# Kernel tuning notes

Measured on AMD Instinct MI355X. Metric: run time of the kernel, lower is better.

## Reference

```python
import jax, jax.numpy as jnp
import numpy as np

SR = 44100.0  # sample_rate from init_kwargs


def _alpha(tau_ms):
    # Eq. (10): alpha = exp(-1 / (tau_s * fs)), tau clamped to [0.1, 1000] ms
    tau_s = jnp.clip(tau_ms, 0.1, 1000.0) / 1000.0
    return jnp.exp(-1.0 / (tau_s * SR))


def _env(x, alpha, attack):
    # Nonlinear envelope follower (Eqs. 9-10).
    # attack=True  -> smooth attack (when |x| rising), instant decay
    # attack=False -> smooth decay  (when |x| falling), instant attack
    xa = jnp.abs(x)
    xs = jnp.moveaxis(xa, -1, 0)  # [T, B, C]
    y0 = jnp.zeros(xa.shape[:-1], xa.dtype)  # [B, C]

    def step(y_prev, xn):
        cond = (xn > y_prev) if attack else (xn < y_prev)
        y_curr = jnp.where(cond, (1.0 - alpha) * xn + alpha * y_prev, xn)
        return y_curr, y_curr

    _, ys = jax.lax.scan(step, y0, xs)
    return jnp.moveaxis(ys, 0, -1)  # [B, C, T]


def _db_to_amp(db):
    return jnp.power(10.0, db / 20.0)


def reference(x, tauAtc, tauDtc, nu, dBregDelta):
    # Temporal Contrast Enhancement (Weger et al., ICAD 2019, Eqs. 12-14).
    # high_pass_filter is the identity in the source, so sh = x.
    alpha_d = _alpha(jnp.clip(tauDtc, 1.0, 100.0))
    alpha_a = _alpha(jnp.clip(tauAtc, 1.0, 100.0))
    et_d = _env(x, alpha_d, attack=False)      # envd(sh)
    et_a = _env(et_d, alpha_a, attack=True)    # enva(et_d)
    nu_amp = _db_to_amp(jnp.clip(nu, -60.0, 0.0))
    et = jnp.maximum(et_d - et_a - nu_amp, 0.0)
    et_env = _env(et, alpha_d, attack=False)   # envd(et)
    reg = _db_to_amp(jnp.clip(dBregDelta, -120.0, -60.0))
    modulation = et / (et_env + reg)
    return x * modulation


def setup_inputs() -> dict:
    key = jax.random.key(0)
    x = jax.random.normal(key, (8, 32, 88200), dtype=jnp.float32)  # [B, C, T]
    return {
        "x": x,
        "tauAtc": jnp.float32(3.0),
        "tauDtc": jnp.float32(7.0),
        "nu": jnp.float32(-40.0),
        "dBregDelta": jnp.float32(-96.0),
    }
```

## Files before the change

### kernel.cpp

```cpp
#include <hip/hip_runtime.h>
#include <cmath>


static constexpr int   kT  = 88200;
static constexpr float kSR = 44100.0f;

struct EnvP { float ad, bd, aa, ba, nuamp, reg; };

__device__ __forceinline__ EnvP make_params(const float* tauA, const float* tauD,
                                            const float* nu, const float* dbreg) {
  EnvP p;
  float td = fminf(fmaxf(tauD[0], 1.0f), 100.0f);
  td = fminf(fmaxf(td, 0.1f), 1000.0f) * 0.001f;
  float ta = fminf(fmaxf(tauA[0], 1.0f), 100.0f);
  ta = fminf(fmaxf(ta, 0.1f), 1000.0f) * 0.001f;
  p.ad = expf(-1.0f / (td * kSR));
  p.aa = expf(-1.0f / (ta * kSR));
  p.bd = 1.0f - p.ad;
  p.ba = 1.0f - p.aa;
  p.nuamp = exp10f(fminf(fmaxf(nu[0],    -60.0f),   0.0f) * 0.05f);
  p.reg   = exp10f(fminf(fmaxf(dbreg[0], -120.0f), -60.0f) * 0.05f);
  return p;
}

template <int S, int MODE>
__global__ __launch_bounds__(256)
void k_pass(const float* __restrict__ x,
            const float* tauA, const float* tauD,
            const float* nu, const float* dbreg,
            const float* __restrict__ Yd, const float* __restrict__ Ya,
            const float* __restrict__ Ye,
            float* __restrict__ O0, float* __restrict__ O1) {
  constexpr int PADS = S + 4;
  __shared__ float lds[256 * PADS];
  const int t   = threadIdx.x;
  const int blk = blockIdx.x;
  const size_t tileBase = (size_t)blk * (256 * S);
  const float4* xg = reinterpret_cast<const float4*>(x + tileBase);

#pragma unroll
  for (int i = 0; i < S / 4; ++i) {
    int idx = t + i * 256;
    float4 v = xg[idx];
    int chunk = (idx * 4) / S;
    int off   = idx * 4 - chunk * S;
    *reinterpret_cast<float4*>(&lds[chunk * PADS + off]) = v;
  }
  __syncthreads();

  EnvP p = make_params(tauA, tauD, nu, dbreg);
  const int gchunk = blk * 256 + t;
  float* my = &lds[t * PADS];

  if (MODE == 0) {
    float A = -INFINITY, B = 0.0f;
#pragma unroll 2
    for (int i = 0; i < S / 4; ++i) {
      float4 v = *reinterpret_cast<const float4*>(&my[4 * i]);
      float vv[4] = {v.x, v.y, v.z, v.w};
#pragma unroll
      for (int j = 0; j < 4; ++j) {
        float xa = fabsf(vv[j]);
        float bx = p.bd * xa;
        A = fmaxf(xa, fmaf(p.ad, A, bx));
        B = fmaf(p.ad, B, bx);
      }
    }
    O0[gchunk] = A; O1[gchunk] = B;
  } else if (MODE == 1) {
    float yd = Yd[gchunk];
    float A = INFINITY, B = 0.0f;
#pragma unroll 2
    for (int i = 0; i < S / 4; ++i) {
      float4 v = *reinterpret_cast<const float4*>(&my[4 * i]);
      float vv[4] = {v.x, v.y, v.z, v.w};
#pragma unroll
      for (int j = 0; j < 4; ++j) {
        float xa = fabsf(vv[j]);
        yd = fmaxf(xa, fmaf(p.ad, yd, p.bd * xa));
        float by = p.ba * yd;
        A = fminf(yd, fmaf(p.aa, A, by));
        B = fmaf(p.aa, B, by);
      }
    }
    O0[gchunk] = A; O1[gchunk] = B;
  } else if (MODE == 2) {
    float yd = Yd[gchunk], ya = Ya[gchunk];
    float A = -INFINITY, B = 0.0f;
#pragma unroll 2
    for (int i = 0; i < S / 4; ++i) {
      float4 v = *reinterpret_cast<const float4*>(&my[4 * i]);
      float vv[4] = {v.x, v.y, v.z, v.w};
#pragma unroll
      for (int j = 0; j < 4; ++j) {
        float xa = fabsf(vv[j]);
        yd = fmaxf(xa, fmaf(p.ad, yd, p.bd * xa));
        ya = fminf(yd, fmaf(p.aa, ya, p.ba * yd));
        float et = fmaxf((yd - ya) - p.nuamp, 0.0f);
        float bx = p.bd * et;
        A = fmaxf(et, fmaf(p.ad, A, bx));
        B = fmaf(p.ad, B, bx);
      }
    }
    O0[gchunk] = A; O1[gchunk] = B;
  } else {
    float yd = Yd[gchunk], ya = Ya[gchunk], ye = Ye[gchunk];
#pragma unroll 2
    for (int i = 0; i < S / 4; ++i) {
      float4 v = *reinterpret_cast<const float4*>(&my[4 * i]);
      float vv[4] = {v.x, v.y, v.z, v.w};
      float oo[4];
#pragma unroll
      for (int j = 0; j < 4; ++j) {
        float xa = fabsf(vv[j]);
        yd = fmaxf(xa, fmaf(p.ad, yd, p.bd * xa));
        ya = fminf(yd, fmaf(p.aa, ya, p.ba * yd));
        float et = fmaxf((yd - ya) - p.nuamp, 0.0f);
        ye = fmaxf(et, fmaf(p.ad, ye, p.bd * et));
        oo[j] = vv[j] * (et / (ye + p.reg));
      }
      *reinterpret_cast<float4*>(&my[4 * i]) = make_float4(oo[0], oo[1], oo[2], oo[3]);
    }
    __syncthreads();
    float4* og = reinterpret_cast<float4*>(O0 + tileBase);
#pragma unroll
    for (int i = 0; i < S / 4; ++i) {
      int idx = t + i * 256;
      int chunk = (idx * 4) / S;
      int off   = idx * 4 - chunk * S;
      og[idx] = *reinterpret_cast<const float4*>(&lds[chunk * PADS + off]);
    }
  }
}

template <int S, int ATTACK>
__global__ __launch_bounds__(256)
void k_scan(const float* __restrict__ A, const float* __restrict__ B,
            float* __restrict__ Y,
            const float* tauA, const float* tauD,
            const float* nu, const float* dbreg) {
  constexpr int NC  = kT / S;
  constexpr int CPT = (NC + 255) / 256;
  EnvP p = make_params(tauA, tauD, nu, dbreg);
  const float alpha = ATTACK ? p.aa : p.ad;
  const float ID_A  = ATTACK ? INFINITY : -INFINITY;
  int s = blockIdx.x, t = threadIdx.x;
  long base = (long)s * NC;
  float gS = powf(alpha, (float)S);

  float ca[CPT], cb[CPT];
  float a = ID_A, b = 0.0f, g = 1.0f;
#pragma unroll
  for (int k = 0; k < CPT; ++k) {
    int c = t * CPT + k;
    if (c < NC) { ca[k] = A[base + c]; cb[k] = B[base + c]; }
    else        { ca[k] = ID_A;        cb[k] = 0.0f; }
    float cg = (c < NC) ? gS : 1.0f;
    float na = ATTACK ? fminf(ca[k], fmaf(cg, a, cb[k]))
                      : fmaxf(ca[k], fmaf(cg, a, cb[k]));
    b = fmaf(cg, b, cb[k]);
    g = cg * g;
    a = na;
  }

  __shared__ float sA[256], sB[256], sG[256];
  sA[t] = a; sB[t] = b; sG[t] = g;
  __syncthreads();
#pragma unroll
  for (int d = 1; d < 256; d <<= 1) {
    float pa = 0.0f, pb = 0.0f, pg = 0.0f;
    if (t >= d) { pa = sA[t - d]; pb = sB[t - d]; pg = sG[t - d]; }
    __syncthreads();
    if (t >= d) {
      float na = ATTACK ? fminf(a, fmaf(g, pa, b)) : fmaxf(a, fmaf(g, pa, b));
      b = fmaf(g, pb, b);
      g = g * pg;
      a = na;
      sA[t] = a; sB[t] = b; sG[t] = g;
    }
    __syncthreads();
  }

  float ea, eb;
  if (t == 0) { ea = ID_A; eb = 0.0f; }
  else        { ea = sA[t - 1]; eb = sB[t - 1]; }

#pragma unroll
  for (int k = 0; k < CPT; ++k) {
    int c = t * CPT + k;
    if (c >= NC) break;
    Y[base + c] = ATTACK ? fminf(ea, eb) : fmaxf(ea, eb);
    float na = ATTACK ? fminf(ca[k], fmaf(gS, ea, cb[k]))
                      : fmaxf(ca[k], fmaf(gS, ea, cb[k]));
    eb = fmaf(gS, eb, cb[k]);
    ea = na;
  }
}

template <int S>
static void run_pipeline(const float* x, const float* tauA, const float* tauD,
                         const float* nu, const float* dbreg, float* out,
                         float* wsf, int nseries, hipStream_t stream) {
  const int nc  = kT / S;
  const int nch = nseries * nc;
  float* A  = wsf;
  float* B  = wsf + (size_t)nch;
  float* Yd = wsf + (size_t)2 * nch;
  float* Ya = wsf + (size_t)3 * nch;
  float* Ye = wsf + (size_t)4 * nch;
  const int grid = nch / 256;

  k_pass<S, 0><<<grid, 256, 0, stream>>>(x, tauA, tauD, nu, dbreg, nullptr, nullptr, nullptr, A, B);
  k_scan<S, 0><<<nseries, 256, 0, stream>>>(A, B, Yd, tauA, tauD, nu, dbreg);
  k_pass<S, 1><<<grid, 256, 0, stream>>>(x, tauA, tauD, nu, dbreg, Yd, nullptr, nullptr, A, B);
  k_scan<S, 1><<<nseries, 256, 0, stream>>>(A, B, Ya, tauA, tauD, nu, dbreg);
  k_pass<S, 2><<<grid, 256, 0, stream>>>(x, tauA, tauD, nu, dbreg, Yd, Ya, nullptr, A, B);
  k_scan<S, 0><<<nseries, 256, 0, stream>>>(A, B, Ye, tauA, tauD, nu, dbreg);
  k_pass<S, 3><<<grid, 256, 0, stream>>>(x, tauA, tauD, nu, dbreg, Yd, Ya, Ye, out, nullptr);
}

extern "C" void kernel_launch(void* const* d_in, const int* in_sizes, int n_in,
                              void* d_out, int out_size, void* d_ws, size_t ws_size,
                              hipStream_t stream) {
  const float* x     = (const float*)d_in[0];
  const float* tauA  = (const float*)d_in[1];
  const float* tauD  = (const float*)d_in[2];
  const float* nu    = (const float*)d_in[3];
  const float* dbreg = (const float*)d_in[4];
  float* out = (float*)d_out;
  float* wsf = (float*)d_ws;
  int nseries = in_sizes[0] / kT;

  auto fits = [&](int S) {
    return (size_t)5 * nseries * (kT / S) * sizeof(float) <= ws_size;
  };
  if      (fits(40))  run_pipeline<40>(x, tauA, tauD, nu, dbreg, out, wsf, nseries, stream);
  else if (fits(56))  run_pipeline<56 >(x, tauA, tauD, nu, dbreg, out, wsf, nseries, stream);
  else if (fits(72))  run_pipeline<72 >(x, tauA, tauD, nu, dbreg, out, wsf, nseries, stream);
  else                run_pipeline<120>(x, tauA, tauD, nu, dbreg, out, wsf, nseries, stream);
}
```

Before: 235.0 us.

## Fuse seven-kernel scan pipeline into single-pass decoupled-lookback kernel

Replaces the four pass kernels and three scan kernels with one persistent-style kernel. Each block takes a dynamic tile id from an atomic ticket, loads its tile of x into LDS once, and for each of the three envelope stages does a block scan, publishes the tile aggregate, and walks the flags of earlier tiles to get its carry-in. This removes the repeated global re-reads of x, the intermediate workspace traffic and the launch gaps. In exchange it adds a memset, serial spin-waiting on predecessor tiles (three chained lookbacks per tile, with a linear walk from tile 0), and a guard timeout that could silently produce wrong carries if a predecessor stalls.

```diff
diff --git a/kernel.cpp b/kernel.cpp
--- a/kernel.cpp
+++ b/kernel.cpp
@@ -2,8 +2,14 @@
 #include <cmath>
 
 
-static constexpr int   kT  = 88200;
-static constexpr float kSR = 44100.0f;
+static constexpr int   kT   = 88200;
+static constexpr float kSR  = 44100.0f;
+static constexpr int   kS   = 40;
+static constexpr int   kS4  = kS / 4;
+static constexpr int   kNC  = kT / kS;
+static constexpr int   kCT  = 256;
+static constexpr int   kNT  = (kNC + kCT - 1) / kCT;
+static constexpr int   kPad = kS + 4;
 
 struct EnvP { float ad, bd, aa, ba, nuamp, reg; };
 
@@ -23,39 +29,119 @@
   return p;
 }
 
-template <int S, int MODE>
+template <int ATTACK>
+__device__ __forceinline__ void block_scan(float a, float b, float g,
+                                           float* sA, float* sB, float* sG, int t) {
+  sA[t] = a; sB[t] = b; sG[t] = g;
+  __syncthreads();
+#pragma unroll
+  for (int d = 1; d < 256; d <<= 1) {
+    float pa = 0.f, pb = 0.f, pg = 0.f;
+    bool has = (t >= d);
+    if (has) { pa = sA[t - d]; pb = sB[t - d]; pg = sG[t - d]; }
+    __syncthreads();
+    if (has) {
+      float na = ATTACK ? fminf(a, fmaf(g, pa, b)) : fmaxf(a, fmaf(g, pa, b));
+      b = fmaf(g, pb, b);
+      g = g * pg;
+      a = na;
+      sA[t] = a; sB[t] = b; sG[t] = g;
+    }
+    __syncthreads();
+  }
+}
+
 __global__ __launch_bounds__(256)
-void k_pass(const float* __restrict__ x,
-            const float* tauA, const float* tauD,
-            const float* nu, const float* dbreg,
-            const float* __restrict__ Yd, const float* __restrict__ Ya,
-            const float* __restrict__ Ye,
-            float* __restrict__ O0, float* __restrict__ O1) {
-  constexpr int PADS = S + 4;
-  __shared__ float lds[256 * PADS];
-  const int t   = threadIdx.x;
-  const int blk = blockIdx.x;
-  const size_t tileBase = (size_t)blk * (256 * S);
-  const float4* xg = reinterpret_cast<const float4*>(x + tileBase);
-
-#pragma unroll
-  for (int i = 0; i < S / 4; ++i) {
-    int idx = t + i * 256;
+void k_fused(const float* __restrict__ x,
+             const float* tauA, const float* tauD,
+             const float* nu, const float* dbreg,
+             float* __restrict__ out,
+             unsigned* __restrict__ tick,
+             unsigned* __restrict__ flags,
+             float*    __restrict__ aggs,
+             int nseries) {
+  __shared__ float lds[kCT * kPad];
+  __shared__ float sA[256], sB[256], sG[256];
+  __shared__ float sIn;
+  __shared__ unsigned sVid;
+
+  const int t = threadIdx.x;
+  if (t == 0) sVid = atomicAdd(tick, 1u);
+  __syncthreads();
+  const int vid  = (int)sVid;
+  const int tile = vid / nseries;
+  const int s    = vid - tile * nseries;
+  const int NTILES = nseries * kNT;
+  const int nchunks = min(kCT, kNC - tile * kCT);
+  const int n4 = (nchunks * kS) >> 2;
+  const size_t gbase = (size_t)s * kT + (size_t)tile * (kCT * kS);
+
+  const float4* xg = reinterpret_cast<const float4*>(x + gbase);
+  for (int idx = t; idx < n4; idx += 256) {
     float4 v = xg[idx];
-    int chunk = (idx * 4) / S;
-    int off   = idx * 4 - chunk * S;
-    *reinterpret_cast<float4*>(&lds[chunk * PADS + off]) = v;
-  }
-  __syncthreads();
-
-  EnvP p = make_params(tauA, tauD, nu, dbreg);
-  const int gchunk = blk * 256 + t;
-  float* my = &lds[t * PADS];
-
-  if (MODE == 0) {
-    float A = -INFINITY, B = 0.0f;
-#pragma unroll 2
-    for (int i = 0; i < S / 4; ++i) {
+    int chunk = idx / kS4;
+    int off   = (idx - chunk * kS4) * 4;
+    *reinterpret_cast<float4*>(&lds[chunk * kPad + off]) = v;
+  }
+  __syncthreads();
+
+  const EnvP p = make_params(tauA, tauD, nu, dbreg);
+  const bool act = (t < nchunks);
+  const float* my = &lds[t * kPad];
+  const float gSd = powf(p.ad, (float)kS);
+  const float gSa = powf(p.aa, (float)kS);
+
+  float* aggA[3]; float* aggB[3]; float* aggG[3];
+#pragma unroll
+  for (int ph = 0; ph < 3; ++ph) {
+    aggA[ph] = aggs + (size_t)(3 * ph + 0) * NTILES;
+    aggB[ph] = aggs + (size_t)(3 * ph + 1) * NTILES;
+    aggG[ph] = aggs + (size_t)(3 * ph + 2) * NTILES;
+  }
+  const int myidx = s * kNT + tile;
+
+  auto publish_and_lookback = [&](int ph, int ATTACK) {
+    if (t == 0) {
+      __hip_atomic_store(&aggA[ph][myidx], sA[255], __ATOMIC_RELAXED, __HIP_MEMORY_SCOPE_AGENT);
+      __hip_atomic_store(&aggB[ph][myidx], sB[255], __ATOMIC_RELAXED, __HIP_MEMORY_SCOPE_AGENT);
+      __hip_atomic_store(&aggG[ph][myidx], sG[255], __ATOMIC_RELAXED, __HIP_MEMORY_SCOPE_AGENT);
+      __hip_atomic_store(&flags[ph * NTILES + myidx], 1u, __ATOMIC_RELEASE, __HIP_MEMORY_SCOPE_AGENT);
+      const float ID_A = ATTACK ? INFINITY : -INFINITY;
+      float ea = ID_A, eb = 0.f, eg = 1.f;
+      for (int k = 0; k < tile; ++k) {
+        int idx = s * kNT + k;
+        unsigned v = 0; int guard = 0;
+        for (;;) {
+          v = __hip_atomic_load(&flags[ph * NTILES + idx], __ATOMIC_ACQUIRE, __HIP_MEMORY_SCOPE_AGENT);
+          if (v || ++guard > (1 << 18)) break;
+          __builtin_amdgcn_s_sleep(8);
+        }
+        float ka = __hip_atomic_load(&aggA[ph][idx], __ATOMIC_RELAXED, __HIP_MEMORY_SCOPE_AGENT);
+        float kb = __hip_atomic_load(&aggB[ph][idx], __ATOMIC_RELAXED, __HIP_MEMORY_SCOPE_AGENT);
+        float kg = __hip_atomic_load(&aggG[ph][idx], __ATOMIC_RELAXED, __HIP_MEMORY_SCOPE_AGENT);
+        float na = ATTACK ? fminf(ka, fmaf(kg, ea, kb)) : fmaxf(ka, fmaf(kg, ea, kb));
+        eb = fmaf(kg, eb, kb);
+        eg = kg * eg;
+        ea = na;
+      }
+      sIn = ATTACK ? fminf(ea, eb) : fmaxf(ea, eb);
+    }
+    __syncthreads();
+  };
+
+  auto chunk_entry = [&](int ATTACK) -> float {
+    float yIn = sIn;
+    float ea, eb, eg;
+    if (t == 0) { ea = ATTACK ? INFINITY : -INFINITY; eb = 0.f; eg = 1.f; }
+    else        { ea = sA[t - 1]; eb = sB[t - 1]; eg = sG[t - 1]; }
+    float v = fmaf(eg, yIn, eb);
+    return ATTACK ? fminf(ea, v) : fmaxf(ea, v);
+  };
+
+  float A = -INFINITY, B = 0.f, G = act ? gSd : 1.f;
+  if (act) {
+#pragma unroll
+    for (int i = 0; i < kS4; ++i) {
       float4 v = *reinterpret_cast<const float4*>(&my[4 * i]);
       float vv[4] = {v.x, v.y, v.z, v.w};
 #pragma unroll
@@ -66,12 +152,17 @@
         B = fmaf(p.ad, B, bx);
       }
     }
-    O0[gchunk] = A; O1[gchunk] = B;
-  } else if (MODE == 1) {
-    float yd = Yd[gchunk];
-    float A = INFINITY, B = 0.0f;
-#pragma unroll 2
-    for (int i = 0; i < S / 4; ++i) {
+  }
+  block_scan<0>(A, B, G, sA, sB, sG, t);
+  publish_and_lookback(0, 0);
+  const float yd0 = chunk_entry(0);
+  __syncthreads();
+
+  A = INFINITY; B = 0.f; G = act ? gSa : 1.f;
+  if (act) {
+    float yd = yd0;
+#pragma unroll
+    for (int i = 0; i < kS4; ++i) {
       float4 v = *reinterpret_cast<const float4*>(&my[4 * i]);
       float vv[4] = {v.x, v.y, v.z, v.w};
 #pragma unroll
@@ -83,12 +174,17 @@
         B = fmaf(p.aa, B, by);
       }
     }
-    O0[gchunk] = A; O1[gchunk] = B;
-  } else if (MODE == 2) {
-    float yd = Yd[gchunk], ya = Ya[gchunk];
-    float A = -INFINITY, B = 0.0f;
-#pragma unroll 2
-    for (int i = 0; i < S / 4; ++i) {
+  }
+  block_scan<1>(A, B, G, sA, sB, sG, t);
+  publish_and_lookback(1, 1);
+  const float ya0 = chunk_entry(1);
+  __syncthreads();
+
+  A = -INFINITY; B = 0.f; G = act ? gSd : 1.f;
+  if (act) {
+    float yd = yd0, ya = ya0;
+#pragma unroll
+    for (int i = 0; i < kS4; ++i) {
       float4 v = *reinterpret_cast<const float4*>(&my[4 * i]);
       float vv[4] = {v.x, v.y, v.z, v.w};
 #pragma unroll
@@ -102,12 +198,18 @@
         B = fmaf(p.ad, B, bx);
       }
     }
-    O0[gchunk] = A; O1[gchunk] = B;
-  } else {
-    float yd = Yd[gchunk], ya = Ya[gchunk], ye = Ye[gchunk];
-#pragma unroll 2
-    for (int i = 0; i < S / 4; ++i) {
-      float4 v = *reinterpret_cast<const float4*>(&my[4 * i]);
+  }
+  block_scan<0>(A, B, G, sA, sB, sG, t);
+  publish_and_lookback(2, 0);
+  const float ye0 = chunk_entry(0);
+  __syncthreads();
+
+  if (act) {
+    float yd = yd0, ya = ya0, ye = ye0;
+    float* myw = &lds[t * kPad];
+#pragma unroll
+    for (int i = 0; i < kS4; ++i) {
+      float4 v = *reinterpret_cast<const float4*>(&myw[4 * i]);
       float vv[4] = {v.x, v.y, v.z, v.w};
       float oo[4];
 #pragma unroll
@@ -119,104 +221,16 @@
         ye = fmaxf(et, fmaf(p.ad, ye, p.bd * et));
         oo[j] = vv[j] * (et / (ye + p.reg));
       }
-      *reinterpret_cast<float4*>(&my[4 * i]) = make_float4(oo[0], oo[1], oo[2], oo[3]);
-    }
-    __syncthreads();
-    float4* og = reinterpret_cast<float4*>(O0 + tileBase);
-#pragma unroll
-    for (int i = 0; i < S / 4; ++i) {
-      int idx = t + i * 256;
-      int chunk = (idx * 4) / S;
-      int off   = idx * 4 - chunk * S;
-      og[idx] = *reinterpret_cast<const float4*>(&lds[chunk * PADS + off]);
-    }
-  }
-}
-
-template <int S, int ATTACK>
-__global__ __launch_bounds__(256)
-void k_scan(const float* __restrict__ A, const float* __restrict__ B,
-            float* __restrict__ Y,
-            const float* tauA, const float* tauD,
-            const float* nu, const float* dbreg) {
-  constexpr int NC  = kT / S;
-  constexpr int CPT = (NC + 255) / 256;
-  EnvP p = make_params(tauA, tauD, nu, dbreg);
-  const float alpha = ATTACK ? p.aa : p.ad;
-  const float ID_A  = ATTACK ? INFINITY : -INFINITY;
-  int s = blockIdx.x, t = threadIdx.x;
-  long base = (long)s * NC;
-  float gS = powf(alpha, (float)S);
-
-  float ca[CPT], cb[CPT];
-  float a = ID_A, b = 0.0f, g = 1.0f;
-#pragma unroll
-  for (int k = 0; k < CPT; ++k) {
-    int c = t * CPT + k;
-    if (c < NC) { ca[k] = A[base + c]; cb[k] = B[base + c]; }
-    else        { ca[k] = ID_A;        cb[k] = 0.0f; }
-    float cg = (c < NC) ? gS : 1.0f;
-    float na = ATTACK ? fminf(ca[k], fmaf(cg, a, cb[k]))
-                      : fmaxf(ca[k], fmaf(cg, a, cb[k]));
-    b = fmaf(cg, b, cb[k]);
-    g = cg * g;
-    a = na;
-  }
-
-  __shared__ float sA[256], sB[256], sG[256];
-  sA[t] = a; sB[t] = b; sG[t] = g;
-  __syncthreads();
-#pragma unroll
-  for (int d = 1; d < 256; d <<= 1) {
-    float pa = 0.0f, pb = 0.0f, pg = 0.0f;
-    if (t >= d) { pa = sA[t - d]; pb = sB[t - d]; pg = sG[t - d]; }
-    __syncthreads();
-    if (t >= d) {
-      float na = ATTACK ? fminf(a, fmaf(g, pa, b)) : fmaxf(a, fmaf(g, pa, b));
-      b = fmaf(g, pb, b);
-      g = g * pg;
-      a = na;
-      sA[t] = a; sB[t] = b; sG[t] = g;
-    }
-    __syncthreads();
-  }
-
-  float ea, eb;
-  if (t == 0) { ea = ID_A; eb = 0.0f; }
-  else        { ea = sA[t - 1]; eb = sB[t - 1]; }
-
-#pragma unroll
-  for (int k = 0; k < CPT; ++k) {
-    int c = t * CPT + k;
-    if (c >= NC) break;
-    Y[base + c] = ATTACK ? fminf(ea, eb) : fmaxf(ea, eb);
-    float na = ATTACK ? fminf(ca[k], fmaf(gS, ea, cb[k]))
-                      : fmaxf(ca[k], fmaf(gS, ea, cb[k]));
-    eb = fmaf(gS, eb, cb[k]);
-    ea = na;
-  }
-}
-
-template <int S>
-static void run_pipeline(const float* x, const float* tauA, const float* tauD,
-                         const float* nu, const float* dbreg, float* out,
-                         float* wsf, int nseries, hipStream_t stream) {
-  const int nc  = kT / S;
-  const int nch = nseries * nc;
-  float* A  = wsf;
-  float* B  = wsf + (size_t)nch;
-  float* Yd = wsf + (size_t)2 * nch;
-  float* Ya = wsf + (size_t)3 * nch;
-  float* Ye = wsf + (size_t)4 * nch;
-  const int grid = nch / 256;
-
-  k_pass<S, 0><<<grid, 256, 0, stream>>>(x, tauA, tauD, nu, dbreg, nullptr, nullptr, nullptr, A, B);
-  k_scan<S, 0><<<nseries, 256, 0, stream>>>(A, B, Yd, tauA, tauD, nu, dbreg);
-  k_pass<S, 1><<<grid, 256, 0, stream>>>(x, tauA, tauD, nu, dbreg, Yd, nullptr, nullptr, A, B);
-  k_scan<S, 1><<<nseries, 256, 0, stream>>>(A, B, Ya, tauA, tauD, nu, dbreg);
-  k_pass<S, 2><<<grid, 256, 0, stream>>>(x, tauA, tauD, nu, dbreg, Yd, Ya, nullptr, A, B);
-  k_scan<S, 0><<<nseries, 256, 0, stream>>>(A, B, Ye, tauA, tauD, nu, dbreg);
-  k_pass<S, 3><<<grid, 256, 0, stream>>>(x, tauA, tauD, nu, dbreg, Yd, Ya, Ye, out, nullptr);
+      *reinterpret_cast<float4*>(&myw[4 * i]) = make_float4(oo[0], oo[1], oo[2], oo[3]);
+    }
+  }
+  __syncthreads();
+  float4* og = reinterpret_cast<float4*>(out + gbase);
+  for (int idx = t; idx < n4; idx += 256) {
+    int chunk = idx / kS4;
+    int off   = (idx - chunk * kS4) * 4;
+    og[idx] = *reinterpret_cast<const float4*>(&lds[chunk * kPad + off]);
+  }
 }
 
 extern "C" void kernel_launch(void* const* d_in, const int* in_sizes, int n_in,
@@ -228,14 +242,16 @@
   const float* nu    = (const float*)d_in[3];
   const float* dbreg = (const float*)d_in[4];
   float* out = (float*)d_out;
-  float* wsf = (float*)d_ws;
-  int nseries = in_sizes[0] / kT;
-
-  auto fits = [&](int S) {
-    return (size_t)5 * nseries * (kT / S) * sizeof(float) <= ws_size;
-  };
-  if      (fits(40))  run_pipeline<40>(x, tauA, tauD, nu, dbreg, out, wsf, nseries, stream);
-  else if (fits(56))  run_pipeline<56 >(x, tauA, tauD, nu, dbreg, out, wsf, nseries, stream);
-  else if (fits(72))  run_pipeline<72 >(x, tauA, tauD, nu, dbreg, out, wsf, nseries, stream);
-  else                run_pipeline<120>(x, tauA, tauD, nu, dbreg, out, wsf, nseries, stream);
-}
+
+  const int nseries = in_sizes[0] / kT;
+  const int NTILES  = nseries * kNT;
+
+  unsigned* tick  = (unsigned*)d_ws;
+  unsigned* flags = tick + 1;
+  float*    aggs  = (float*)(flags + (size_t)3 * NTILES);
+
+  hipMemsetAsync(d_ws, 0, sizeof(unsigned) * (1 + (size_t)3 * NTILES), stream);
+
+  k_fused<<<NTILES, 256, 0, stream>>>(x, tauA, tauD, nu, dbreg, out,
+                                      tick, flags, aggs, nseries);
+}
```

After: 550.9 us. +134.5%, slower.

## Fuse seven-launch scan pipeline into one cooperative kernel with grid syncs

Applied to the files above, without the earlier changes.

Replaces the seven separate pass/scan kernel launches with a single cooperative persistent kernel that loops over tiles and uses grid-wide syncs between phases. The aim is to remove launch gaps and the tail cost of the tiny per-series scan kernels. The trade-offs are a grid capped by occupancy, so each block handles several tiles serially, and the scan phases use only 256 blocks while the rest wait at the grid barrier. It also drops the workspace-size fallback and fixes S=40, and adds host-side occupancy and device-property queries on every call.

```diff
diff --git a/kernel.cpp b/kernel.cpp
--- a/kernel.cpp
+++ b/kernel.cpp
@@ -1,9 +1,17 @@
 #include <hip/hip_runtime.h>
+#include <hip/hip_cooperative_groups.h>
 #include <cmath>
 
-
-static constexpr int   kT  = 88200;
-static constexpr float kSR = 44100.0f;
+namespace cg = cooperative_groups;
+
+
+static constexpr int   kT   = 88200;
+static constexpr float kSR  = 44100.0f;
+static constexpr int   kS   = 40;
+static constexpr int   kS4  = kS / 4;
+static constexpr int   kNC  = kT / kS;
+static constexpr int   kCT  = 256;
+static constexpr int   kPad = kS + 4;
 
 struct EnvP { float ad, bd, aa, ba, nuamp, reg; };
 
@@ -23,39 +31,30 @@
   return p;
 }
 
-template <int S, int MODE>
-__global__ __launch_bounds__(256)
-void k_pass(const float* __restrict__ x,
-            const float* tauA, const float* tauD,
-            const float* nu, const float* dbreg,
-            const float* __restrict__ Yd, const float* __restrict__ Ya,
-            const float* __restrict__ Ye,
-            float* __restrict__ O0, float* __restrict__ O1) {
-  constexpr int PADS = S + 4;
-  __shared__ float lds[256 * PADS];
-  const int t   = threadIdx.x;
-  const int blk = blockIdx.x;
-  const size_t tileBase = (size_t)blk * (256 * S);
+template <int MODE>
+__device__ __forceinline__ void comp_tile(int g, int t,
+    const float* __restrict__ x, float* lds, const EnvP& p,
+    const float* __restrict__ Yd, const float* __restrict__ Ya,
+    const float* __restrict__ Ye,
+    float* __restrict__ O0, float* __restrict__ O1) {
+  const size_t tileBase = (size_t)g * (kCT * kS);
   const float4* xg = reinterpret_cast<const float4*>(x + tileBase);
-
-#pragma unroll
-  for (int i = 0; i < S / 4; ++i) {
+#pragma unroll
+  for (int i = 0; i < kS4; ++i) {
     int idx = t + i * 256;
     float4 v = xg[idx];
-    int chunk = (idx * 4) / S;
-    int off   = idx * 4 - chunk * S;
-    *reinterpret_cast<float4*>(&lds[chunk * PADS + off]) = v;
+    int chunk = idx / kS4;
+    int off   = (idx - chunk * kS4) * 4;
+    *reinterpret_cast<float4*>(&lds[chunk * kPad + off]) = v;
   }
   __syncthreads();
-
-  EnvP p = make_params(tauA, tauD, nu, dbreg);
-  const int gchunk = blk * 256 + t;
-  float* my = &lds[t * PADS];
+  const int gchunk = g * kCT + t;
+  float* my = &lds[t * kPad];
 
   if (MODE == 0) {
-    float A = -INFINITY, B = 0.0f;
+    float A = -INFINITY, B = 0.f;
 #pragma unroll 2
-    for (int i = 0; i < S / 4; ++i) {
+    for (int i = 0; i < kS4; ++i) {
       float4 v = *reinterpret_cast<const float4*>(&my[4 * i]);
       float vv[4] = {v.x, v.y, v.z, v.w};
 #pragma unroll
@@ -69,9 +68,9 @@
     O0[gchunk] = A; O1[gchunk] = B;
   } else if (MODE == 1) {
     float yd = Yd[gchunk];
-    float A = INFINITY, B = 0.0f;
+    float A = INFINITY, B = 0.f;
 #pragma unroll 2
-    for (int i = 0; i < S / 4; ++i) {
+    for (int i = 0; i < kS4; ++i) {
       float4 v = *reinterpret_cast<const float4*>(&my[4 * i]);
       float vv[4] = {v.x, v.y, v.z, v.w};
 #pragma unroll
@@ -86,9 +85,9 @@
     O0[gchunk] = A; O1[gchunk] = B;
   } else if (MODE == 2) {
     float yd = Yd[gchunk], ya = Ya[gchunk];
-    float A = -INFINITY, B = 0.0f;
+    float A = -INFINITY, B = 0.f;
 #pragma unroll 2
-    for (int i = 0; i < S / 4; ++i) {
+    for (int i = 0; i < kS4; ++i) {
       float4 v = *reinterpret_cast<const float4*>(&my[4 * i]);
       float vv[4] = {v.x, v.y, v.z, v.w};
 #pragma unroll
@@ -106,7 +105,7 @@
   } else {
     float yd = Yd[gchunk], ya = Ya[gchunk], ye = Ye[gchunk];
 #pragma unroll 2
-    for (int i = 0; i < S / 4; ++i) {
+    for (int i = 0; i < kS4; ++i) {
       float4 v = *reinterpret_cast<const float4*>(&my[4 * i]);
       float vv[4] = {v.x, v.y, v.z, v.w};
       float oo[4];
@@ -124,51 +123,48 @@
     __syncthreads();
     float4* og = reinterpret_cast<float4*>(O0 + tileBase);
 #pragma unroll
-    for (int i = 0; i < S / 4; ++i) {
+    for (int i = 0; i < kS4; ++i) {
       int idx = t + i * 256;
-      int chunk = (idx * 4) / S;
-      int off   = idx * 4 - chunk * S;
-      og[idx] = *reinterpret_cast<const float4*>(&lds[chunk * PADS + off]);
-    }
-  }
-}
-
-template <int S, int ATTACK>
-__global__ __launch_bounds__(256)
-void k_scan(const float* __restrict__ A, const float* __restrict__ B,
-            float* __restrict__ Y,
-            const float* tauA, const float* tauD,
-            const float* nu, const float* dbreg) {
-  constexpr int NC  = kT / S;
+      int chunk = idx / kS4;
+      int off   = (idx - chunk * kS4) * 4;
+      og[idx] = *reinterpret_cast<const float4*>(&lds[chunk * kPad + off]);
+    }
+  }
+  __syncthreads();
+}
+
+template <int ATTACK>
+__device__ __forceinline__ void scan_series(const float* __restrict__ A,
+                                            const float* __restrict__ B,
+                                            float* __restrict__ Y,
+                                            int s, int t, const EnvP& p,
+                                            float* sA, float* sB, float* sG) {
+  constexpr int NC  = kNC;
   constexpr int CPT = (NC + 255) / 256;
-  EnvP p = make_params(tauA, tauD, nu, dbreg);
   const float alpha = ATTACK ? p.aa : p.ad;
   const float ID_A  = ATTACK ? INFINITY : -INFINITY;
-  int s = blockIdx.x, t = threadIdx.x;
   long base = (long)s * NC;
-  float gS = powf(alpha, (float)S);
+  float gS = powf(alpha, (float)kS);
 
   float ca[CPT], cb[CPT];
-  float a = ID_A, b = 0.0f, g = 1.0f;
+  float a = ID_A, b = 0.f, g = 1.f;
 #pragma unroll
   for (int k = 0; k < CPT; ++k) {
     int c = t * CPT + k;
     if (c < NC) { ca[k] = A[base + c]; cb[k] = B[base + c]; }
-    else        { ca[k] = ID_A;        cb[k] = 0.0f; }
-    float cg = (c < NC) ? gS : 1.0f;
+    else        { ca[k] = ID_A;        cb[k] = 0.f; }
+    float cg = (c < NC) ? gS : 1.f;
     float na = ATTACK ? fminf(ca[k], fmaf(cg, a, cb[k]))
                       : fmaxf(ca[k], fmaf(cg, a, cb[k]));
     b = fmaf(cg, b, cb[k]);
     g = cg * g;
     a = na;
   }
-
-  __shared__ float sA[256], sB[256], sG[256];
   sA[t] = a; sB[t] = b; sG[t] = g;
   __syncthreads();
 #pragma unroll
   for (int d = 1; d < 256; d <<= 1) {
-    float pa = 0.0f, pb = 0.0f, pg = 0.0f;
+    float pa = 0.f, pb = 0.f, pg = 0.f;
     if (t >= d) { pa = sA[t - d]; pb = sB[t - d]; pg = sG[t - d]; }
     __syncthreads();
     if (t >= d) {
@@ -180,11 +176,9 @@
     }
     __syncthreads();
   }
-
   float ea, eb;
-  if (t == 0) { ea = ID_A; eb = 0.0f; }
+  if (t == 0) { ea = ID_A; eb = 0.f; }
   else        { ea = sA[t - 1]; eb = sB[t - 1]; }
-
 #pragma unroll
   for (int k = 0; k < CPT; ++k) {
     int c = t * CPT + k;
@@ -195,28 +189,65 @@
     eb = fmaf(gS, eb, cb[k]);
     ea = na;
   }
-}
-
-template <int S>
-static void run_pipeline(const float* x, const float* tauA, const float* tauD,
-                         const float* nu, const float* dbreg, float* out,
-                         float* wsf, int nseries, hipStream_t stream) {
-  const int nc  = kT / S;
-  const int nch = nseries * nc;
-  float* A  = wsf;
-  float* B  = wsf + (size_t)nch;
-  float* Yd = wsf + (size_t)2 * nch;
-  float* Ya = wsf + (size_t)3 * nch;
-  float* Ye = wsf + (size_t)4 * nch;
-  const int grid = nch / 256;
-
-  k_pass<S, 0><<<grid, 256, 0, stream>>>(x, tauA, tauD, nu, dbreg, nullptr, nullptr, nullptr, A, B);
-  k_scan<S, 0><<<nseries, 256, 0, stream>>>(A, B, Yd, tauA, tauD, nu, dbreg);
-  k_pass<S, 1><<<grid, 256, 0, stream>>>(x, tauA, tauD, nu, dbreg, Yd, nullptr, nullptr, A, B);
-  k_scan<S, 1><<<nseries, 256, 0, stream>>>(A, B, Ya, tauA, tauD, nu, dbreg);
-  k_pass<S, 2><<<grid, 256, 0, stream>>>(x, tauA, tauD, nu, dbreg, Yd, Ya, nullptr, A, B);
-  k_scan<S, 0><<<nseries, 256, 0, stream>>>(A, B, Ye, tauA, tauD, nu, dbreg);
-  k_pass<S, 3><<<grid, 256, 0, stream>>>(x, tauA, tauD, nu, dbreg, Yd, Ya, Ye, out, nullptr);
+  __syncthreads();
+}
+
+__global__ __launch_bounds__(256, 3)
+void k_coop(const float* __restrict__ x,
+            const float* tauA, const float* tauD,
+            const float* nu, const float* dbreg,
+            float* __restrict__ out,
+            float* __restrict__ A, float* __restrict__ B,
+            float* __restrict__ Yd, float* __restrict__ Ya,
+            float* __restrict__ Ye,
+            int nseries, int ntiles) {
+  cg::grid_group grid = cg::this_grid();
+  __shared__ float lds[kCT * kPad];
+  __shared__ float sA[256], sB[256], sG[256];
+  const int t = threadIdx.x;
+  const EnvP p = make_params(tauA, tauD, nu, dbreg);
+
+  for (int g = blockIdx.x; g < ntiles; g += gridDim.x)
+    comp_tile<0>(g, t, x, lds, p, nullptr, nullptr, nullptr, A, B);
+  grid.sync();
+  if (blockIdx.x < nseries) scan_series<0>(A, B, Yd, blockIdx.x, t, p, sA, sB, sG);
+  grid.sync();
+  for (int g = blockIdx.x; g < ntiles; g += gridDim.x)
+    comp_tile<1>(g, t, x, lds, p, Yd, nullptr, nullptr, A, B);
+  grid.sync();
+  if (blockIdx.x < nseries) scan_series<1>(A, B, Ya, blockIdx.x, t, p, sA, sB, sG);
+  grid.sync();
+  for (int g = blockIdx.x; g < ntiles; g += gridDim.x)
+    comp_tile<2>(g, t, x, lds, p, Yd, Ya, nullptr, A, B);
+  grid.sync();
+  if (blockIdx.x < nseries) scan_series<0>(A, B, Ye, blockIdx.x, t, p, sA, sB, sG);
+  grid.sync();
+  for (int g = blockIdx.x; g < ntiles; g += gridDim.x)
+    comp_tile<3>(g, t, x, lds, p, Yd, Ya, Ye, out, nullptr);
+}
+
+template <int MODE>
+__global__ __launch_bounds__(256)
+void k_pass(const float* __restrict__ x,
+            const float* tauA, const float* tauD,
+            const float* nu, const float* dbreg,
+            const float* __restrict__ Yd, const float* __restrict__ Ya,
+            const float* __restrict__ Ye,
+            float* __restrict__ O0, float* __restrict__ O1) {
+  __shared__ float lds[kCT * kPad];
+  EnvP p = make_params(tauA, tauD, nu, dbreg);
+  comp_tile<MODE>(blockIdx.x, threadIdx.x, x, lds, p, Yd, Ya, Ye, O0, O1);
+}
+
+template <int ATTACK>
+__global__ __launch_bounds__(256)
+void k_scan(const float* __restrict__ A, const float* __restrict__ B,
+            float* __restrict__ Y,
+            const float* tauA, const float* tauD,
+            const float* nu, const float* dbreg) {
+  __shared__ float sA[256], sB[256], sG[256];
+  EnvP p = make_params(tauA, tauD, nu, dbreg);
+  scan_series<ATTACK>(A, B, Y, blockIdx.x, threadIdx.x, p, sA, sB, sG);
 }
 
 extern "C" void kernel_launch(void* const* d_in, const int* in_sizes, int n_in,
@@ -228,14 +259,45 @@
   const float* nu    = (const float*)d_in[3];
   const float* dbreg = (const float*)d_in[4];
   float* out = (float*)d_out;
+
+  int nseries = in_sizes[0] / kT;
+  int nch     = nseries * kNC;
+  int ntiles  = nch / kCT;
+
   float* wsf = (float*)d_ws;
-  int nseries = in_sizes[0] / kT;
-
-  auto fits = [&](int S) {
-    return (size_t)5 * nseries * (kT / S) * sizeof(float) <= ws_size;
-  };
-  if      (fits(40))  run_pipeline<40>(x, tauA, tauD, nu, dbreg, out, wsf, nseries, stream);
-  else if (fits(56))  run_pipeline<56 >(x, tauA, tauD, nu, dbreg, out, wsf, nseries, stream);
-  else if (fits(72))  run_pipeline<72 >(x, tauA, tauD, nu, dbreg, out, wsf, nseries, stream);
-  else                run_pipeline<120>(x, tauA, tauD, nu, dbreg, out, wsf, nseries, stream);
-}
+  float* A  = wsf;
+  float* B  = wsf + (size_t)nch;
+  float* Yd = wsf + (size_t)2 * nch;
+  float* Ya = wsf + (size_t)3 * nch;
+  float* Ye = wsf + (size_t)4 * nch;
+
+  int occ = 0;
+  hipOccupancyMaxActiveBlocksPerMultiprocessor(&occ, k_coop, 256, 0);
+  if (occ < 1) occ = 1;
+  int numCU = 256;
+  hipDeviceProp_t prop;
+  int dev = 0;
+  if (hipGetDevice(&dev) == hipSuccess &&
+      hipGetDeviceProperties(&prop, dev) == hipSuccess)
+    numCU = prop.multiProcessorCount;
+  int grid = occ * numCU;
+  if (grid > ntiles) grid = ntiles;
+  if (grid < nseries) grid = nseries;
+
+  void* args[] = {(void*)&x, (void*)&tauA, (void*)&tauD, (void*)&nu,
+                  (void*)&dbreg, (void*)&out, (void*)&A, (void*)&B,
+                  (void*)&Yd, (void*)&Ya, (void*)&Ye,
+                  (void*)&nseries, (void*)&ntiles};
+  hipError_t err = hipLaunchCooperativeKernel((const void*)k_coop,
+                                              dim3(grid), dim3(256),
+                                              args, 0, stream);
+  if (err != hipSuccess) {
+    k_pass<0><<<ntiles, 256, 0, stream>>>(x, tauA, tauD, nu, dbreg, nullptr, nullptr, nullptr, A, B);
+    k_scan<0><<<nseries, 256, 0, stream>>>(A, B, Yd, tauA, tauD, nu, dbreg);
+    k_pass<1><<<ntiles, 256, 0, stream>>>(x, tauA, tauD, nu, dbreg, Yd, nullptr, nullptr, A, B);
+    k_scan<1><<<nseries, 256, 0, stream>>>(A, B, Ya, tauA, tauD, nu, dbreg);
+    k_pass<2><<<ntiles, 256, 0, stream>>>(x, tauA, tauD, nu, dbreg, Yd, Ya, nullptr, A, B);
+    k_scan<0><<<nseries, 256, 0, stream>>>(A, B, Ye, tauA, tauD, nu, dbreg);
+    k_pass<3><<<ntiles, 256, 0, stream>>>(x, tauA, tauD, nu, dbreg, Yd, Ya, Ye, out, nullptr);
+  }
+}
```

After: 716.4 us. +204.9%, slower.
